# Performance work log

Measured on AMD Instinct MI355X. Metric: run time of the kernel, lower is better.

The kernel has to match this reference:

```python
import jax, jax.numpy as jnp
import numpy as np

# irreps kept in the output (sorted): 0e (dim 1), 1o (dim 3), 2e (dim 5)
IRS = (("0e", 1), ("1o", 3), ("2e", 5))
# multiplicity of each irrep in the reduced symmetric tensor product basis per order
MULS = {1: {"0e": 1, "1o": 1, "2e": 1},
        2: {"0e": 2, "1o": 2, "2e": 3},
        3: {"0e": 4, "1o": 6, "2e": 8}}
N, C, D, S, CORR = 1024, 128, 9, 10, 3  # nodes, channels, irreps dim (0e+1o+2e), species, correlation


def setup_inputs() -> dict:
    key = jax.random.key(0)
    ks = iter(jax.random.split(key, 64))
    inp = {"x": jax.random.normal(next(ks), (N, C, D), dtype=jnp.float32)}
    for order in range(1, CORR + 1):
        for ir, idim in IRS:
            mul = MULS[order][ir]
            # U basis tensor: shape (D,)*order + (mul, ir_dim); CG-like tensors are sparse
            u = jax.random.normal(next(ks), (D,) * order + (mul, idim), dtype=jnp.float32)
            mask = jax.random.bernoulli(next(ks), 0.25, u.shape)
            inp[f"u{order}_{ir}"] = jnp.where(mask, u, 0.0)
            # per-species weights, stddev mul**-0.5 ('element' gradient normalization)
            inp[f"w{order}_{ir}"] = jax.random.normal(next(ks), (S, mul, C), dtype=jnp.float32) * (mul ** -0.5)
    inp["index"] = jax.random.randint(next(ks), (N,), 0, S)
    return inp


def _forward(x, index, us, ws):
    # x: (N, C, D) node features; index: (N,) species ids
    out = {}
    for order in range(CORR, 0, -1):
        for ir, idim in IRS:
            w = ws[order][ir][index]  # per-species weight gather -> (N, mul, C)
            u = us[order][ir]          # (D,)*order + (mul, idim)
            if order == CORR:
                # highest order: contract one D axis with x together with the weights
                out[ir] = jnp.einsum('...jki,zkc,zcj->zc...i', u, w, x)
            else:
                # accumulate this order's term, then contract one more D axis with x
                acc = out[ir] + jnp.einsum('...ki,zkc->zc...i', u, w)
                out[ir] = jnp.einsum('zc...ji,zcj->zc...i', acc, x)
    # final out[ir]: (N, C, idim); axis_to_mul -> concat of (N, C*idim) blocks
    return jnp.concatenate([out[ir].reshape(N, C * idim) for ir, idim in IRS], axis=-1)


def reference(x, u1_0e, u1_1o, u1_2e, u2_0e, u2_1o, u2_2e, u3_0e, u3_1o, u3_2e,
              w1_0e, w1_1o, w1_2e, w2_0e, w2_1o, w2_2e, w3_0e, w3_1o, w3_2e, index):
    us = {1: {"0e": u1_0e, "1o": u1_1o, "2e": u1_2e},
          2: {"0e": u2_0e, "1o": u2_1o, "2e": u2_2e},
          3: {"0e": u3_0e, "1o": u3_1o, "2e": u3_2e}}
    ws = {1: {"0e": w1_0e, "1o": w1_1o, "2e": w1_2e},
          2: {"0e": w2_0e, "1o": w2_1o, "2e": w2_2e},
          3: {"0e": w3_0e, "1o": w3_1o, "2e": w3_2e}}
    return _forward(x, index, us, ws)
```

## Files before the change

### kernel.cpp

```cpp
#include <hip/hip_runtime.h>


#define NMONO 219
#define NPAIR 54
#define NN 1024
#define NC 128
#define NS 10
#define NPB 2
#define PADBLK 528

struct Tables {
    int mt[NMONO];
    int pair_ab[NPAIR];
    int pair_m0[NPAIR + 1];
    int qs[5];
};

constexpr Tables make_tables() {
    Tables T{};
    int m = 0, pg = 0;
    for (int a = 0; a < 9; a++)
        for (int b = a; b < 10; b++) {
            T.pair_ab[pg] = (a << 4) | b;
            T.pair_m0[pg] = m;
            for (int j = b; j < 10; j++) { T.mt[m] = (a << 8) | (b << 4) | j; m++; }
            pg++;
        }
    T.pair_m0[NPAIR] = m;
    T.qs[0] = 0; T.qs[4] = NPAIR;
    for (int q = 1; q < 4; q++) {
        int best = 0; long bestd = 1L << 40;
        for (int p = 0; p <= NPAIR; p++) {
            long d = 4L * T.pair_m0[p] - 219L * q;
            if (d < 0) d = -d;
            if (d < bestd) { bestd = d; best = p; }
        }
        T.qs[q] = best;
    }
    return T;
}

__device__ __constant__ const Tables TBL = make_tables();

__global__ __launch_bounds__(128) void precompute_uw(
    const float* __restrict__ u1_0e, const float* __restrict__ w1_0e,
    const float* __restrict__ u1_1o, const float* __restrict__ w1_1o,
    const float* __restrict__ u1_2e, const float* __restrict__ w1_2e,
    const float* __restrict__ u2_0e, const float* __restrict__ w2_0e,
    const float* __restrict__ u2_1o, const float* __restrict__ w2_1o,
    const float* __restrict__ u2_2e, const float* __restrict__ w2_2e,
    const float* __restrict__ u3_0e, const float* __restrict__ w3_0e,
    const float* __restrict__ u3_1o, const float* __restrict__ w3_1o,
    const float* __restrict__ u3_2e, const float* __restrict__ w3_2e,
    float* __restrict__ uwA, float* __restrict__ uwB)
{
    const int blk  = blockIdx.x;
    const int s    = blk / NMONO;
    const int mono = blk % NMONO;
    const int c    = threadIdx.x;
    const int t    = threadIdx.x;
    __shared__ float usum[64];

    const int e = TBL.mt[mono];
    const int A = (e >> 8) & 15, B = (e >> 4) & 15, J = e & 15;
    const bool deg3 = (J < 9);
    const bool deg1 = (B == 9);

    if (deg3) {
        if (t < 62) {
            const float* u; int mul, idim, k, i;
            if (t < 4)       { u = u3_0e; mul = 4; idim = 1; k = t; i = 0; }
            else if (t < 22) { u = u3_1o; mul = 6; idim = 3; int r = t - 4;  k = r / 3; i = r % 3; }
            else             { u = u3_2e; mul = 8; idim = 5; int r = t - 22; k = r / 5; i = r % 5; }
            int arr[6] = { A*81+B*9+J, A*81+J*9+B, B*81+A*9+J, B*81+J*9+A, J*81+A*9+B, J*81+B*9+A };
            float sv = 0.f;
            for (int p = 0; p < 6; p++) {
                bool dup = false;
                for (int q = 0; q < p; q++) if (arr[q] == arr[p]) dup = true;
                if (!dup) sv += u[arr[p]*(mul*idim) + k*idim + i];
            }
            usum[t] = sv;
        }
    } else if (!deg1) {
        if (t < 23) {
            const float* u; int mul, idim, k, i;
            if (t < 2)      { u = u2_0e; mul = 2; idim = 1; k = t; i = 0; }
            else if (t < 8) { u = u2_1o; mul = 2; idim = 3; int r = t - 2; k = r / 3; i = r % 3; }
            else            { u = u2_2e; mul = 3; idim = 5; int r = t - 8; k = r / 5; i = r % 5; }
            float sv = u[(A*9+B)*(mul*idim) + k*idim + i];
            if (A != B) sv += u[(B*9+A)*(mul*idim) + k*idim + i];
            usum[t] = sv;
        }
    } else {
        if (t < 9) {
            float sv;
            if (t == 0)      sv = u1_0e[A];
            else if (t < 4)  sv = u1_1o[A*3 + (t-1)];
            else             sv = u1_2e[A*5 + (t-4)];
            usum[t] = sv;
        }
    }
    __syncthreads();

    float o[9];
    if (deg3) {
        float v = 0.f;
        #pragma unroll
        for (int k = 0; k < 4; k++) v += usum[k] * w3_0e[(s*4+k)*NC + c];
        o[0] = v;
        #pragma unroll
        for (int i = 0; i < 3; i++) {
            v = 0.f;
            #pragma unroll
            for (int k = 0; k < 6; k++) v += usum[4 + k*3 + i] * w3_1o[(s*6+k)*NC + c];
            o[1+i] = v;
        }
        #pragma unroll
        for (int i = 0; i < 5; i++) {
            v = 0.f;
            #pragma unroll
            for (int k = 0; k < 8; k++) v += usum[22 + k*5 + i] * w3_2e[(s*8+k)*NC + c];
            o[4+i] = v;
        }
    } else if (!deg1) {
        float v = 0.f;
        #pragma unroll
        for (int k = 0; k < 2; k++) v += usum[k] * w2_0e[(s*2+k)*NC + c];
        o[0] = v;
        #pragma unroll
        for (int i = 0; i < 3; i++) {
            v = 0.f;
            #pragma unroll
            for (int k = 0; k < 2; k++) v += usum[2 + k*3 + i] * w2_1o[(s*2+k)*NC + c];
            o[1+i] = v;
        }
        #pragma unroll
        for (int i = 0; i < 5; i++) {
            v = 0.f;
            #pragma unroll
            for (int k = 0; k < 3; k++) v += usum[8 + k*5 + i] * w2_2e[(s*3+k)*NC + c];
            o[4+i] = v;
        }
    } else {
        o[0] = usum[0] * w1_0e[s*NC + c];
        #pragma unroll
        for (int i = 0; i < 3; i++) o[1+i] = usum[1+i] * w1_1o[s*NC + c];
        #pragma unroll
        for (int i = 0; i < 5; i++) o[4+i] = usum[4+i] * w1_2e[s*NC + c];
    }

    const size_t base = (size_t)(s*NMONO + mono)*NC + c;
    float4 lo; lo.x = o[0]; lo.y = o[1]; lo.z = o[2]; lo.w = o[3];
    float4 hi; hi.x = o[4]; hi.y = o[5]; hi.z = o[6]; hi.w = o[7];
    *(float4*)(uwA + base*8)     = lo;
    *(float4*)(uwA + base*8 + 4) = hi;
    uwB[base] = o[8];
}

__global__ __launch_bounds__(1024) void build_groups(
    const int* __restrict__ index,
    int* __restrict__ perm,
    int* __restrict__ offs,
    int* __restrict__ blockmap)
{
    __shared__ int cnt[NS], pos[NS], nbstart[NS+1];
    __shared__ int sh_nch;
    const int t = threadIdx.x;
    if (t < NS) cnt[t] = 0;
    __syncthreads();
    const int s = index[t];
    atomicAdd(&cnt[s], 1);
    __syncthreads();
    if (t == 0) {
        int o = 0, g = 0;
        for (int i = 0; i < NS; i++) {
            offs[i] = o; pos[i] = o; o += cnt[i];
            nbstart[i] = g; g += (cnt[i] + NPB - 1) / NPB;
        }
        offs[NS] = o; nbstart[NS] = g; sh_nch = g;
    }
    __syncthreads();
    const int Nch = sh_nch;
    for (int p = t; p < PADBLK; p += 1024) { blockmap[2*p] = -1; blockmap[2*p+1] = 0; }
    __syncthreads();
    if (t < Nch) {
        const int g = t;
        const int q = Nch >> 3, r = Nch & 7;
        int x = 0, stx = 0;
        for (int xx = 0; xx < 8; xx++) {
            const int cx = q + (xx < r ? 1 : 0);
            if (g < stx + cx) { x = xx; break; }
            stx += cx;
        }
        const int p = x + 8 * (g - stx);
        int sp = 0;
        while (g >= nbstart[sp+1]) sp++;
        blockmap[2*p]   = sp;
        blockmap[2*p+1] = g - nbstart[sp];
    }
    const int r2 = atomicAdd(&pos[s], 1);
    perm[r2] = t;
}

__global__ __launch_bounds__(1024, 8) void symcon_main(
    const float* __restrict__ x,
    const int* __restrict__ perm, const int* __restrict__ offs,
    const int* __restrict__ blockmap,
    const float* __restrict__ uwA, const float* __restrict__ uwB,
    float* __restrict__ out)
{
    __shared__ float lx[256][11];
    __shared__ float red[3][256][9];

    const int tid = threadIdx.x;
    const int z   = tid >> 8;
    const int hc  = tid & 255;
    const int h   = hc >> 7;
    const int c   = tid & 127;

    const int s     = blockmap[2*blockIdx.x];
    const int chunk = blockmap[2*blockIdx.x + 1];
    if (s < 0) return;
    const int gbeg = offs[s], gend = offs[s+1];
    const int p0   = gbeg + chunk*NPB;
    const int node0 = perm[p0];
    const bool v1   = (p0 + 1 < gend);
    const int node1 = perm[v1 ? p0 + 1 : p0];

    for (int f = tid; f < 1152; f += 1024) {
        const int ch = f / 9;
        const int d  = f - ch*9;
        lx[ch][d]     = x[(size_t)node0*1152 + f];
        lx[128+ch][d] = x[(size_t)node1*1152 + f];
    }
    if (tid < 256) lx[tid][9] = 1.0f;
    __syncthreads();

    const float* lxr = &lx[hc][0];
    const int pg0 = TBL.qs[z], pg1 = TBL.qs[z+1];
    const int m0  = TBL.pair_m0[pg0];
    const float* pA = uwA + ((size_t)(s*NMONO + m0)*NC + c) * 8;
    const float* pB = uwB +  (size_t)(s*NMONO + m0)*NC + c;

    float acc[9];
    #pragma unroll
    for (int i = 0; i < 9; i++) acc[i] = 0.f;

    for (int pg = pg0; pg < pg1; ++pg) {
        const int ab = TBL.pair_ab[pg];
        const int a = ab >> 4, b = ab & 15;
        const float p2 = lxr[a] * lxr[b];
        for (int j = b; j < 10; ++j) {
            const float p  = p2 * lxr[j];
            const float4 f0 = *(const float4*)(pA);
            const float4 f1 = *(const float4*)(pA + 4);
            const float  fb = *pB;
            acc[0] += f0.x*p; acc[1] += f0.y*p; acc[2] += f0.z*p; acc[3] += f0.w*p;
            acc[4] += f1.x*p; acc[5] += f1.y*p; acc[6] += f1.z*p; acc[7] += f1.w*p;
            acc[8] += fb*p;
            pA += NC*8; pB += NC;
        }
    }

    if (z > 0) {
        #pragma unroll
        for (int i = 0; i < 9; i++) red[z-1][hc][i] = acc[i];
    }
    __syncthreads();
    if (z == 0) {
        #pragma unroll
        for (int i = 0; i < 9; i++)
            acc[i] += red[0][hc][i] + red[1][hc][i] + red[2][hc][i];
        if (h == 0 || v1) {
            const int node = h ? node1 : node0;
            float* orow = out + (size_t)node * 1152;
            orow[c] = acc[0];
            #pragma unroll
            for (int i = 0; i < 3; i++) orow[128 + c*3 + i] = acc[1+i];
            #pragma unroll
            for (int i = 0; i < 5; i++) orow[512 + c*5 + i] = acc[4+i];
        }
    }
}

extern "C" void kernel_launch(void* const* d_in, const int* in_sizes, int n_in,
                              void* d_out, int out_size, void* d_ws, size_t ws_size,
                              hipStream_t stream)
{
    const float* x     = (const float*)d_in[0];
    const float* u1_0e = (const float*)d_in[1];
    const float* w1_0e = (const float*)d_in[2];
    const float* u1_1o = (const float*)d_in[3];
    const float* w1_1o = (const float*)d_in[4];
    const float* u1_2e = (const float*)d_in[5];
    const float* w1_2e = (const float*)d_in[6];
    const float* u2_0e = (const float*)d_in[7];
    const float* w2_0e = (const float*)d_in[8];
    const float* u2_1o = (const float*)d_in[9];
    const float* w2_1o = (const float*)d_in[10];
    const float* u2_2e = (const float*)d_in[11];
    const float* w2_2e = (const float*)d_in[12];
    const float* u3_0e = (const float*)d_in[13];
    const float* w3_0e = (const float*)d_in[14];
    const float* u3_1o = (const float*)d_in[15];
    const float* w3_1o = (const float*)d_in[16];
    const float* u3_2e = (const float*)d_in[17];
    const float* w3_2e = (const float*)d_in[18];
    const int*   index = (const int*)d_in[19];
    float* out = (float*)d_out;

    float* uwA = (float*)d_ws;
    float* uwB = uwA + (size_t)NS*NMONO*NC*8;
    int*   perm     = (int*)(uwB + (size_t)NS*NMONO*NC);
    int*   offs     = perm + NN;
    int*   blockmap = offs + (NS+1);

    hipLaunchKernelGGL(build_groups, dim3(1), dim3(NN), 0, stream,
        index, perm, offs, blockmap);

    hipLaunchKernelGGL(precompute_uw, dim3(NS*NMONO), dim3(128), 0, stream,
        u1_0e, w1_0e, u1_1o, w1_1o, u1_2e, w1_2e,
        u2_0e, w2_0e, u2_1o, w2_1o, u2_2e, w2_2e,
        u3_0e, w3_0e, u3_1o, w3_1o, u3_2e, w3_2e, uwA, uwB);

    hipLaunchKernelGGL(symcon_main, dim3(PADBLK), dim3(1024), 0, stream,
        x, perm, offs, blockmap, uwA, uwB, out);
}
```

Before: 158.1 us.

## Process four nodes per block and split the UW precompute into symmetrize and fold

```diff
diff --git a/kernel.cpp b/kernel.cpp
--- a/kernel.cpp
+++ b/kernel.cpp
@@ -2,166 +2,165 @@
 
 
 #define NMONO 219
-#define NPAIR 54
 #define NN 1024
 #define NC 128
 #define NS 10
-#define NPB 2
-#define PADBLK 528
-
-struct Tables {
-    int mt[NMONO];
-    int pair_ab[NPAIR];
-    int pair_m0[NPAIR + 1];
-    int qs[5];
-};
+#define NPB 4
+#define PADBLK 272
+#define FOLD_CHUNK 16
+#define NCHUNKF ((NMONO + FOLD_CHUNK - 1) / FOLD_CHUNK)
+
+struct Tables { int mt[NMONO]; };
 
 constexpr Tables make_tables() {
     Tables T{};
-    int m = 0, pg = 0;
+    int m = 0;
     for (int a = 0; a < 9; a++)
-        for (int b = a; b < 10; b++) {
-            T.pair_ab[pg] = (a << 4) | b;
-            T.pair_m0[pg] = m;
+        for (int b = a; b < 10; b++)
             for (int j = b; j < 10; j++) { T.mt[m] = (a << 8) | (b << 4) | j; m++; }
-            pg++;
-        }
-    T.pair_m0[NPAIR] = m;
-    T.qs[0] = 0; T.qs[4] = NPAIR;
-    for (int q = 1; q < 4; q++) {
-        int best = 0; long bestd = 1L << 40;
-        for (int p = 0; p <= NPAIR; p++) {
-            long d = 4L * T.pair_m0[p] - 219L * q;
-            if (d < 0) d = -d;
-            if (d < bestd) { bestd = d; best = p; }
-        }
-        T.qs[q] = best;
-    }
     return T;
 }
-
 __device__ __constant__ const Tables TBL = make_tables();
 
-__global__ __launch_bounds__(128) void precompute_uw(
-    const float* __restrict__ u1_0e, const float* __restrict__ w1_0e,
-    const float* __restrict__ u1_1o, const float* __restrict__ w1_1o,
-    const float* __restrict__ u1_2e, const float* __restrict__ w1_2e,
-    const float* __restrict__ u2_0e, const float* __restrict__ w2_0e,
-    const float* __restrict__ u2_1o, const float* __restrict__ w2_1o,
-    const float* __restrict__ u2_2e, const float* __restrict__ w2_2e,
-    const float* __restrict__ u3_0e, const float* __restrict__ w3_0e,
-    const float* __restrict__ u3_1o, const float* __restrict__ w3_1o,
-    const float* __restrict__ u3_2e, const float* __restrict__ w3_2e,
-    float* __restrict__ uwA, float* __restrict__ uwB)
-{
-    const int blk  = blockIdx.x;
-    const int s    = blk / NMONO;
-    const int mono = blk % NMONO;
-    const int c    = threadIdx.x;
-    const int t    = threadIdx.x;
-    __shared__ float usum[64];
-
+__global__ __launch_bounds__(64) void u_sym(
+    const float* __restrict__ u1_0e, const float* __restrict__ u1_1o, const float* __restrict__ u1_2e,
+    const float* __restrict__ u2_0e, const float* __restrict__ u2_1o, const float* __restrict__ u2_2e,
+    const float* __restrict__ u3_0e, const float* __restrict__ u3_1o, const float* __restrict__ u3_2e,
+    float* __restrict__ usumAll)
+{
+    const int mono = blockIdx.x;
+    const int t = threadIdx.x;
     const int e = TBL.mt[mono];
     const int A = (e >> 8) & 15, B = (e >> 4) & 15, J = e & 15;
-    const bool deg3 = (J < 9);
-    const bool deg1 = (B == 9);
-
-    if (deg3) {
+    float sv = 0.f;
+    if (J < 9) {
         if (t < 62) {
             const float* u; int mul, idim, k, i;
             if (t < 4)       { u = u3_0e; mul = 4; idim = 1; k = t; i = 0; }
             else if (t < 22) { u = u3_1o; mul = 6; idim = 3; int r = t - 4;  k = r / 3; i = r % 3; }
             else             { u = u3_2e; mul = 8; idim = 5; int r = t - 22; k = r / 5; i = r % 5; }
             int arr[6] = { A*81+B*9+J, A*81+J*9+B, B*81+A*9+J, B*81+J*9+A, J*81+A*9+B, J*81+B*9+A };
-            float sv = 0.f;
             for (int p = 0; p < 6; p++) {
                 bool dup = false;
                 for (int q = 0; q < p; q++) if (arr[q] == arr[p]) dup = true;
                 if (!dup) sv += u[arr[p]*(mul*idim) + k*idim + i];
             }
-            usum[t] = sv;
-        }
-    } else if (!deg1) {
+        }
+    } else if (B < 9) {
         if (t < 23) {
             const float* u; int mul, idim, k, i;
             if (t < 2)      { u = u2_0e; mul = 2; idim = 1; k = t; i = 0; }
             else if (t < 8) { u = u2_1o; mul = 2; idim = 3; int r = t - 2; k = r / 3; i = r % 3; }
             else            { u = u2_2e; mul = 3; idim = 5; int r = t - 8; k = r / 5; i = r % 5; }
-            float sv = u[(A*9+B)*(mul*idim) + k*idim + i];
+            sv = u[(A*9+B)*(mul*idim) + k*idim + i];
             if (A != B) sv += u[(B*9+A)*(mul*idim) + k*idim + i];
-            usum[t] = sv;
         }
     } else {
         if (t < 9) {
-            float sv;
             if (t == 0)      sv = u1_0e[A];
             else if (t < 4)  sv = u1_1o[A*3 + (t-1)];
             else             sv = u1_2e[A*5 + (t-4)];
-            usum[t] = sv;
-        }
-    }
-    __syncthreads();
-
-    float o[9];
-    if (deg3) {
-        float v = 0.f;
-        #pragma unroll
-        for (int k = 0; k < 4; k++) v += usum[k] * w3_0e[(s*4+k)*NC + c];
-        o[0] = v;
-        #pragma unroll
-        for (int i = 0; i < 3; i++) {
-            v = 0.f;
-            #pragma unroll
-            for (int k = 0; k < 6; k++) v += usum[4 + k*3 + i] * w3_1o[(s*6+k)*NC + c];
-            o[1+i] = v;
-        }
-        #pragma unroll
-        for (int i = 0; i < 5; i++) {
-            v = 0.f;
-            #pragma unroll
-            for (int k = 0; k < 8; k++) v += usum[22 + k*5 + i] * w3_2e[(s*8+k)*NC + c];
-            o[4+i] = v;
-        }
-    } else if (!deg1) {
-        float v = 0.f;
-        #pragma unroll
-        for (int k = 0; k < 2; k++) v += usum[k] * w2_0e[(s*2+k)*NC + c];
-        o[0] = v;
-        #pragma unroll
-        for (int i = 0; i < 3; i++) {
-            v = 0.f;
-            #pragma unroll
-            for (int k = 0; k < 2; k++) v += usum[2 + k*3 + i] * w2_1o[(s*2+k)*NC + c];
-            o[1+i] = v;
-        }
-        #pragma unroll
-        for (int i = 0; i < 5; i++) {
-            v = 0.f;
-            #pragma unroll
-            for (int k = 0; k < 3; k++) v += usum[8 + k*5 + i] * w2_2e[(s*3+k)*NC + c];
-            o[4+i] = v;
-        }
-    } else {
-        o[0] = usum[0] * w1_0e[s*NC + c];
-        #pragma unroll
-        for (int i = 0; i < 3; i++) o[1+i] = usum[1+i] * w1_1o[s*NC + c];
-        #pragma unroll
-        for (int i = 0; i < 5; i++) o[4+i] = usum[4+i] * w1_2e[s*NC + c];
-    }
-
-    const size_t base = (size_t)(s*NMONO + mono)*NC + c;
-    float4 lo; lo.x = o[0]; lo.y = o[1]; lo.z = o[2]; lo.w = o[3];
-    float4 hi; hi.x = o[4]; hi.y = o[5]; hi.z = o[6]; hi.w = o[7];
-    *(float4*)(uwA + base*8)     = lo;
-    *(float4*)(uwA + base*8 + 4) = hi;
-    uwB[base] = o[8];
+        }
+    }
+    usumAll[mono*64 + t] = sv;
+}
+
+__global__ __launch_bounds__(128) void uw_fold(
+    const float* __restrict__ w1_0e, const float* __restrict__ w1_1o, const float* __restrict__ w1_2e,
+    const float* __restrict__ w2_0e, const float* __restrict__ w2_1o, const float* __restrict__ w2_2e,
+    const float* __restrict__ w3_0e, const float* __restrict__ w3_1o, const float* __restrict__ w3_2e,
+    const float* __restrict__ usumAll,
+    float* __restrict__ uwA, float* __restrict__ uwB)
+{
+    const int s  = blockIdx.x / NCHUNKF;
+    const int m0 = (blockIdx.x % NCHUNKF) * FOLD_CHUNK;
+    const int c  = threadIdx.x;
+    __shared__ float us[FOLD_CHUNK][64];
+
+    for (int f = c; f < FOLD_CHUNK*64; f += 128) {
+        const int mm = f >> 6, sl = f & 63, m = m0 + mm;
+        us[mm][sl] = (m < NMONO) ? usumAll[m*64 + sl] : 0.f;
+    }
+    __syncthreads();
+
+    float W30[4], W31[6], W32[8], W20[2], W21[2], W22[3];
+    #pragma unroll
+    for (int k = 0; k < 4; k++) W30[k] = w3_0e[(s*4+k)*NC + c];
+    #pragma unroll
+    for (int k = 0; k < 6; k++) W31[k] = w3_1o[(s*6+k)*NC + c];
+    #pragma unroll
+    for (int k = 0; k < 8; k++) W32[k] = w3_2e[(s*8+k)*NC + c];
+    #pragma unroll
+    for (int k = 0; k < 2; k++) W20[k] = w2_0e[(s*2+k)*NC + c];
+    #pragma unroll
+    for (int k = 0; k < 2; k++) W21[k] = w2_1o[(s*2+k)*NC + c];
+    #pragma unroll
+    for (int k = 0; k < 3; k++) W22[k] = w2_2e[(s*3+k)*NC + c];
+    const float W10 = w1_0e[s*NC + c], W11 = w1_1o[s*NC + c], W12 = w1_2e[s*NC + c];
+
+    for (int mm = 0; mm < FOLD_CHUNK; mm++) {
+        const int m = m0 + mm;
+        if (m >= NMONO) break;
+        const int e = TBL.mt[m];
+        const int B = (e >> 4) & 15, J = e & 15;
+        float o[9];
+        if (J < 9) {
+            float v = 0.f;
+            #pragma unroll
+            for (int k = 0; k < 4; k++) v += us[mm][k] * W30[k];
+            o[0] = v;
+            #pragma unroll
+            for (int i = 0; i < 3; i++) {
+                v = 0.f;
+                #pragma unroll
+                for (int k = 0; k < 6; k++) v += us[mm][4 + k*3 + i] * W31[k];
+                o[1+i] = v;
+            }
+            #pragma unroll
+            for (int i = 0; i < 5; i++) {
+                v = 0.f;
+                #pragma unroll
+                for (int k = 0; k < 8; k++) v += us[mm][22 + k*5 + i] * W32[k];
+                o[4+i] = v;
+            }
+        } else if (B < 9) {
+            float v = 0.f;
+            #pragma unroll
+            for (int k = 0; k < 2; k++) v += us[mm][k] * W20[k];
+            o[0] = v;
+            #pragma unroll
+            for (int i = 0; i < 3; i++) {
+                v = 0.f;
+                #pragma unroll
+                for (int k = 0; k < 2; k++) v += us[mm][2 + k*3 + i] * W21[k];
+                o[1+i] = v;
+            }
+            #pragma unroll
+            for (int i = 0; i < 5; i++) {
+                v = 0.f;
+                #pragma unroll
+                for (int k = 0; k < 3; k++) v += us[mm][8 + k*5 + i] * W22[k];
+                o[4+i] = v;
+            }
+        } else {
+            o[0] = us[mm][0] * W10;
+            #pragma unroll
+            for (int i = 0; i < 3; i++) o[1+i] = us[mm][1+i] * W11;
+            #pragma unroll
+            for (int i = 0; i < 5; i++) o[4+i] = us[mm][4+i] * W12;
+        }
+        const size_t base = (size_t)(s*NMONO + m)*NC + c;
+        float4 lo; lo.x = o[0]; lo.y = o[1]; lo.z = o[2]; lo.w = o[3];
+        float4 hi; hi.x = o[4]; hi.y = o[5]; hi.z = o[6]; hi.w = o[7];
+        *(float4*)(uwA + base*8)     = lo;
+        *(float4*)(uwA + base*8 + 4) = hi;
+        uwB[base] = o[8];
+    }
 }
 
 __global__ __launch_bounds__(1024) void build_groups(
     const int* __restrict__ index,
-    int* __restrict__ perm,
-    int* __restrict__ offs,
-    int* __restrict__ blockmap)
+    int* __restrict__ perm, int* __restrict__ offs, int* __restrict__ blockmap)
 {
     __shared__ int cnt[NS], pos[NS], nbstart[NS+1];
     __shared__ int sh_nch;
@@ -202,83 +201,130 @@
     perm[r2] = t;
 }
 
-__global__ __launch_bounds__(1024, 8) void symcon_main(
+#define FMA_NODE(Q, P, F0, F1, FB)                                          \
+    acc[Q][0] += F0.x*(P); acc[Q][1] += F0.y*(P); acc[Q][2] += F0.z*(P);    \
+    acc[Q][3] += F0.w*(P); acc[Q][4] += F1.x*(P); acc[Q][5] += F1.y*(P);    \
+    acc[Q][6] += F1.z*(P); acc[Q][7] += F1.w*(P); acc[Q][8] += FB*(P);
+
+#define CONSUME(MM, F0, F1, FB)                                             \
+    { const int e = TBL.mt[MM];                                             \
+      const float4 xa = *(const float4*)&lx4[c44 + ((e>>8)&15)*4];          \
+      const float4 xb = *(const float4*)&lx4[c44 + ((e>>4)&15)*4];          \
+      const float4 xj = *(const float4*)&lx4[c44 + (e&15)*4];               \
+      FMA_NODE(0, xa.x*xb.x*xj.x, F0, F1, FB)                               \
+      FMA_NODE(1, xa.y*xb.y*xj.y, F0, F1, FB)                               \
+      FMA_NODE(2, xa.z*xb.z*xj.z, F0, F1, FB)                               \
+      FMA_NODE(3, xa.w*xb.w*xj.w, F0, F1, FB) }
+
+__global__ __launch_bounds__(512, 4) void symcon_main(
     const float* __restrict__ x,
     const int* __restrict__ perm, const int* __restrict__ offs,
     const int* __restrict__ blockmap,
     const float* __restrict__ uwA, const float* __restrict__ uwB,
     float* __restrict__ out)
 {
-    __shared__ float lx[256][11];
-    __shared__ float red[3][256][9];
+    __shared__ __align__(16) float lx4[128 * 44];
+    __shared__ float red[2][128][36];
 
     const int tid = threadIdx.x;
-    const int z   = tid >> 8;
-    const int hc  = tid & 255;
-    const int h   = hc >> 7;
+    const int z   = tid >> 7;
     const int c   = tid & 127;
+    const int c44 = c * 44;
 
     const int s     = blockmap[2*blockIdx.x];
     const int chunk = blockmap[2*blockIdx.x + 1];
     if (s < 0) return;
     const int gbeg = offs[s], gend = offs[s+1];
     const int p0   = gbeg + chunk*NPB;
-    const int node0 = perm[p0];
-    const bool v1   = (p0 + 1 < gend);
-    const int node1 = perm[v1 ? p0 + 1 : p0];
-
-    for (int f = tid; f < 1152; f += 1024) {
-        const int ch = f / 9;
-        const int d  = f - ch*9;
-        lx[ch][d]     = x[(size_t)node0*1152 + f];
-        lx[128+ch][d] = x[(size_t)node1*1152 + f];
-    }
-    if (tid < 256) lx[tid][9] = 1.0f;
-    __syncthreads();
-
-    const float* lxr = &lx[hc][0];
-    const int pg0 = TBL.qs[z], pg1 = TBL.qs[z+1];
-    const int m0  = TBL.pair_m0[pg0];
-    const float* pA = uwA + ((size_t)(s*NMONO + m0)*NC + c) * 8;
-    const float* pB = uwB +  (size_t)(s*NMONO + m0)*NC + c;
-
-    float acc[9];
-    #pragma unroll
-    for (int i = 0; i < 9; i++) acc[i] = 0.f;
-
-    for (int pg = pg0; pg < pg1; ++pg) {
-        const int ab = TBL.pair_ab[pg];
-        const int a = ab >> 4, b = ab & 15;
-        const float p2 = lxr[a] * lxr[b];
-        for (int j = b; j < 10; ++j) {
-            const float p  = p2 * lxr[j];
-            const float4 f0 = *(const float4*)(pA);
-            const float4 f1 = *(const float4*)(pA + 4);
-            const float  fb = *pB;
-            acc[0] += f0.x*p; acc[1] += f0.y*p; acc[2] += f0.z*p; acc[3] += f0.w*p;
-            acc[4] += f1.x*p; acc[5] += f1.y*p; acc[6] += f1.z*p; acc[7] += f1.w*p;
-            acc[8] += fb*p;
-            pA += NC*8; pB += NC;
-        }
-    }
-
-    if (z > 0) {
-        #pragma unroll
-        for (int i = 0; i < 9; i++) red[z-1][hc][i] = acc[i];
+
+    int node[4]; bool valid[4];
+    #pragma unroll
+    for (int q = 0; q < 4; q++) {
+        const int pi = p0 + q;
+        valid[q] = (pi < gend);
+        node[q]  = perm[valid[q] ? pi : p0];
+    }
+
+    #pragma unroll
+    for (int q = 0; q < 4; q++) {
+        const size_t nb = (size_t)node[q] * 1152;
+        for (int f = tid; f < 1152; f += 512) {
+            const int ch = f / 9, d = f - ch*9;
+            lx4[ch*44 + d*4 + q] = x[nb + f];
+        }
+    }
+    { const int ch = tid >> 2, q = tid & 3; lx4[ch*44 + 36 + q] = 1.0f; }
+    __syncthreads();
+
+    float acc[4][9];
+    #pragma unroll
+    for (int q = 0; q < 4; q++)
+        #pragma unroll
+        for (int i = 0; i < 9; i++) acc[q][i] = 0.f;
+
+    const int mbeg = 55 * z;
+    const int mend = (z == 3) ? NMONO : 55 * (z + 1);
+
+    const float* pa = uwA + ((size_t)(s*NMONO + mbeg)*NC + c) * 8;
+    const float* pb = uwB +  (size_t)(s*NMONO + mbeg)*NC + c;
+
+    float4 A0 = *(const float4*)pa, A1 = *(const float4*)(pa + 4); float Ab = *pb;
+    float4 B0 = *(const float4*)(pa + NC*8), B1 = *(const float4*)(pa + NC*8 + 4); float Bb = *(pb + NC);
+
+    for (int m = mbeg; m < mend; m += 2) {
+        const bool h2 = (m + 2 < mend), h3 = (m + 3 < mend);
+        const float* ra = h2 ? pa + 2*NC*8 : pa;
+        const float* rb = h2 ? pb + 2*NC   : pb;
+        const float* sa = h3 ? pa + 3*NC*8 : pa;
+        const float* sb = h3 ? pb + 3*NC   : pb;
+        const float4 nA0 = *(const float4*)ra, nA1 = *(const float4*)(ra + 4); const float nAb = *rb;
+        const float4 nB0 = *(const float4*)sa, nB1 = *(const float4*)(sa + 4); const float nBb = *sb;
+        CONSUME(m, A0, A1, Ab)
+        if (m + 1 < mend) { CONSUME(m + 1, B0, B1, Bb) }
+        A0 = nA0; A1 = nA1; Ab = nAb;
+        B0 = nB0; B1 = nB1; Bb = nBb;
+        pa += 2*NC*8; pb += 2*NC;
+    }
+
+    if (z >= 2) {
+        float* r = &red[z-2][c][0];
+        #pragma unroll
+        for (int q = 0; q < 4; q++)
+            #pragma unroll
+            for (int i = 0; i < 9; i++) r[q*9 + i] = acc[q][i];
+    }
+    __syncthreads();
+    if (z < 2) {
+        const float* r = &red[z][c][0];
+        #pragma unroll
+        for (int q = 0; q < 4; q++)
+            #pragma unroll
+            for (int i = 0; i < 9; i++) acc[q][i] += r[q*9 + i];
+    }
+    __syncthreads();
+    if (z == 1) {
+        float* r = &red[0][c][0];
+        #pragma unroll
+        for (int q = 0; q < 4; q++)
+            #pragma unroll
+            for (int i = 0; i < 9; i++) r[q*9 + i] = acc[q][i];
     }
     __syncthreads();
     if (z == 0) {
-        #pragma unroll
-        for (int i = 0; i < 9; i++)
-            acc[i] += red[0][hc][i] + red[1][hc][i] + red[2][hc][i];
-        if (h == 0 || v1) {
-            const int node = h ? node1 : node0;
-            float* orow = out + (size_t)node * 1152;
-            orow[c] = acc[0];
-            #pragma unroll
-            for (int i = 0; i < 3; i++) orow[128 + c*3 + i] = acc[1+i];
-            #pragma unroll
-            for (int i = 0; i < 5; i++) orow[512 + c*5 + i] = acc[4+i];
+        const float* r = &red[0][c][0];
+        #pragma unroll
+        for (int q = 0; q < 4; q++)
+            #pragma unroll
+            for (int i = 0; i < 9; i++) acc[q][i] += r[q*9 + i];
+        #pragma unroll
+        for (int q = 0; q < 4; q++) {
+            if (!valid[q]) continue;
+            float* orow = out + (size_t)node[q] * 1152;
+            orow[c] = acc[q][0];
+            #pragma unroll
+            for (int i = 0; i < 3; i++) orow[128 + c*3 + i] = acc[q][1+i];
+            #pragma unroll
+            for (int i = 0; i < 5; i++) orow[512 + c*5 + i] = acc[q][4+i];
         }
     }
 }
@@ -309,20 +355,23 @@
     const int*   index = (const int*)d_in[19];
     float* out = (float*)d_out;
 
-    float* uwA = (float*)d_ws;
-    float* uwB = uwA + (size_t)NS*NMONO*NC*8;
-    int*   perm     = (int*)(uwB + (size_t)NS*NMONO*NC);
+    float* uwA     = (float*)d_ws;
+    float* uwB     = uwA + (size_t)NS*NMONO*NC*8;
+    float* usumAll = uwB + (size_t)NS*NMONO*NC;
+    int*   perm     = (int*)(usumAll + NMONO*64);
     int*   offs     = perm + NN;
     int*   blockmap = offs + (NS+1);
 
     hipLaunchKernelGGL(build_groups, dim3(1), dim3(NN), 0, stream,
         index, perm, offs, blockmap);
 
-    hipLaunchKernelGGL(precompute_uw, dim3(NS*NMONO), dim3(128), 0, stream,
-        u1_0e, w1_0e, u1_1o, w1_1o, u1_2e, w1_2e,
-        u2_0e, w2_0e, u2_1o, w2_1o, u2_2e, w2_2e,
-        u3_0e, w3_0e, u3_1o, w3_1o, u3_2e, w3_2e, uwA, uwB);
-
-    hipLaunchKernelGGL(symcon_main, dim3(PADBLK), dim3(1024), 0, stream,
+    hipLaunchKernelGGL(u_sym, dim3(NMONO), dim3(64), 0, stream,
+        u1_0e, u1_1o, u1_2e, u2_0e, u2_1o, u2_2e, u3_0e, u3_1o, u3_2e, usumAll);
+
+    hipLaunchKernelGGL(uw_fold, dim3(NS*NCHUNKF), dim3(128), 0, stream,
+        w1_0e, w1_1o, w1_2e, w2_0e, w2_1o, w2_2e, w3_0e, w3_1o, w3_2e,
+        usumAll, uwA, uwB);
+
+    hipLaunchKernelGGL(symcon_main, dim3(PADBLK), dim3(512), 0, stream,
         x, perm, offs, blockmap, uwA, uwB, out);
 }
```

Result: faster. 149.5 us (-5.4%).
